# Optimization experiments

Hardware: AMD Instinct MI355X
Metric: run time of the kernel (lower is better)

Reference implementation:

```python
import jax, jax.numpy as jnp
import numpy as np

D_VOC, P_VOC, M_VOC = 2048, 1024, 4096
H = 256
T = 32
LD, LP, LM = 24, 12, 20


def _norm_adj(key, n):
    # binary graph + self loops, row-normalized (matches GCN.normalize(adj+I))
    a = (jax.random.uniform(key, (n, n)) < 0.002).astype(jnp.float32)
    a = a + jnp.eye(n, dtype=jnp.float32)
    rs = a.sum(axis=1)
    rinv = jnp.where(rs > 0, 1.0 / rs, 0.0)
    return rinv[:, None] * a


def setup_inputs() -> dict:
    key = jax.random.key(0)
    ks = jax.random.split(key, 32)
    s = float(1.0 / np.sqrt(H))
    u = lambda k, shape, sc: jax.random.uniform(k, shape, minval=-sc, maxval=sc, dtype=jnp.float32)
    inp = {
        'diag_codes': jax.random.randint(ks[0], (T, LD), 0, D_VOC),
        'proc_codes': jax.random.randint(ks[1], (T, LP), 0, P_VOC),
        'med_codes': jax.random.randint(ks[2], (T - 1, LM), 0, M_VOC),
        'diag_emb': u(ks[3], (D_VOC, H), 0.1),
        'proc_emb': u(ks[4], (P_VOC, H), 0.1),
        'gru_d_wih': u(ks[5], (3 * H, H), s), 'gru_d_whh': u(ks[6], (3 * H, H), s),
        'gru_d_bih': u(ks[7], (3 * H,), s), 'gru_d_bhh': u(ks[8], (3 * H,), s),
        'gru_p_wih': u(ks[9], (3 * H, H), s), 'gru_p_whh': u(ks[10], (3 * H, H), s),
        'gru_p_bih': u(ks[11], (3 * H,), s), 'gru_p_bhh': u(ks[12], (3 * H,), s),
        'q_w': u(ks[13], (2 * H, H), s), 'q_b': u(ks[14], (H,), s),
        'adj_ehr': _norm_adj(ks[15], M_VOC),
        'adj_ddi': _norm_adj(ks[16], M_VOC),
        'w1_ehr': u(ks[17], (M_VOC, H), s), 'b1_ehr': u(ks[18], (H,), s),
        'w2_ehr': u(ks[19], (H, H), s), 'b2_ehr': u(ks[20], (H,), s),
        'w1_ddi': u(ks[21], (M_VOC, H), s), 'b1_ddi': u(ks[22], (H,), s),
        'w2_ddi': u(ks[23], (H, H), s), 'b2_ddi': u(ks[24], (H,), s),
        'inter': jax.random.normal(ks[25], (1,), dtype=jnp.float32) / H,
        'proj_w': u(ks[26], (2 * H, H), s), 'proj_b': u(ks[27], (H,), s),
    }
    return inp


def _gru(x, wih, whh, bih, bhh):
    # torch.nn.GRU cell math; x: [T, H] -> outputs [T, H]
    def step(h, xt):
        gi = xt @ wih.T + bih
        gh = h @ whh.T + bhh
        ir, iz, inn = jnp.split(gi, 3)
        hr, hz, hn = jnp.split(gh, 3)
        r = jax.nn.sigmoid(ir + hr)
        z = jax.nn.sigmoid(iz + hz)
        n = jnp.tanh(inn + r * hn)
        h2 = (1.0 - z) * n + z * h
        return h2, h2
    _, ys = jax.lax.scan(step, jnp.zeros((x.shape[-1],), x.dtype), x)
    return ys


def _gcn(adj, w1, b1, w2, b2):
    # input features are identity, so first support mm(I, w1) == w1
    h1 = jax.nn.relu(adj @ w1 + b1)
    return adj @ (h1 @ w2) + b2


def reference(diag_codes, proc_codes, med_codes, diag_emb, proc_emb,
              gru_d_wih, gru_d_whh, gru_d_bih, gru_d_bhh,
              gru_p_wih, gru_p_whh, gru_p_bih, gru_p_bhh,
              q_w, q_b, adj_ehr, adj_ddi,
              w1_ehr, b1_ehr, w2_ehr, b2_ehr,
              w1_ddi, b1_ddi, w2_ddi, b2_ddi,
              inter, proj_w, proj_b):
    # ---- PatientEncoder: gather + sum codes per visit, GRU over visits ----
    seq_d = diag_emb[diag_codes].sum(axis=1)            # [T, H]
    seq_p = proc_emb[proc_codes].sum(axis=1)            # [T, H]
    od = _gru(seq_d, gru_d_wih, gru_d_whh, gru_d_bih, gru_d_bhh)
    op = _gru(seq_p, gru_p_wih, gru_p_whh, gru_p_bih, gru_p_bhh)
    feats = jnp.concatenate([od, op], axis=-1)          # [T, 2H]
    queries = jax.nn.relu(feats) @ q_w + q_b            # [T, H] (Sequential(ReLU, Linear))
    query = queries[-1:]                                # [1, H]
    history_keys = queries[:-1]                         # [T-1, H]
    # multi-hot history medication values (scatter)
    tm1 = med_codes.shape[0]
    history_values = jnp.zeros((tm1, M_VOC), jnp.float32).at[
        jnp.arange(tm1)[:, None], med_codes].set(1.0)   # [T-1, M_VOC]
    # ---- PriorEncoder ----
    prior = _gcn(adj_ehr, w1_ehr, b1_ehr, w2_ehr, b2_ehr) \
        - inter[0] * _gcn(adj_ddi, w1_ddi, b1_ddi, w2_ddi, b2_ddi)  # [M_VOC, H]
    w_emb = jax.nn.softmax(query @ prior.T, axis=-1)    # [1, M_VOC]
    # diag(w) @ prior == broadcast row-scale (the fused gather-weighted-scale)
    gc1 = w_emb.reshape(-1, 1) * prior                  # [M_VOC, H]
    visit_w = jax.nn.softmax(query @ history_keys.T, axis=-1)  # [1, T-1]
    wv = (visit_w @ history_values).reshape(-1, 1)      # [M_VOC, 1]
    gc2 = wv * prior                                    # [M_VOC, H]
    return jnp.concatenate([gc1, gc2], axis=-1) @ proj_w + proj_b  # [M_VOC, H]
```

## Files before the change

kernel.cpp:

```cpp
#include <hip/hip_runtime.h>
#include <hip/hip_bf16.h>

#define HD   256
#define TT   32
#define MV   4096
#define LD_  24
#define LP_  12
#define LM_  20
#define MAXNZ 96

typedef _Float16 h2v __attribute__((ext_vector_type(2)));
typedef _Float16 h8  __attribute__((ext_vector_type(8)));

__device__ __forceinline__ float fdot2(h2v a, h2v b, float c) {
#if __has_builtin(__builtin_amdgcn_fdot2)
  return __builtin_amdgcn_fdot2(a, b, c, false);
#else
  return c + (float)a[0] * (float)b[0] + (float)a[1] * (float)b[1];
#endif
}

#define PIN2(x) { float _t = __builtin_bit_cast(float, x); \
                  asm volatile("" : "+v"(_t));             \
                  x = __builtin_bit_cast(h2v, _t); }

__global__ __launch_bounds__(768) void k0_cvt(
    const float* __restrict__ whh_d, const float* __restrict__ whh_p,
    h8* __restrict__ wt)
{
  const int i = blockIdx.x, b = blockIdx.y, g = threadIdx.x;
  const float* whh = b ? whh_p : whh_d;
  const float* src = whh + (size_t)g * HD + 8 * i;
  h8 v;
#pragma unroll
  for (int e = 0; e < 8; ++e) v[e] = (_Float16)src[e];
  wt[((size_t)b * 32 + i) * 768 + g] = v;
}

__global__ __launch_bounds__(768) void k1_embed_gi(
    const int* __restrict__ dc, const int* __restrict__ pc,
    const float* __restrict__ demb, const float* __restrict__ pemb,
    const float* __restrict__ wih_d, const float* __restrict__ bih_d,
    const float* __restrict__ wih_p, const float* __restrict__ bih_p,
    float* __restrict__ GI)
{
  const int t = blockIdx.x, b = blockIdx.y;
  const int* codes = b ? pc : dc;
  const int L = b ? LP_ : LD_;
  const float* emb = b ? pemb : demb;
  const float* wih = b ? wih_p : wih_d;
  const float* bih = b ? bih_p : bih_d;
  __shared__ float s[HD];
  const int j = threadIdx.x;
  if (j < HD) {
    float acc = 0.f;
    for (int l = 0; l < L; ++l) acc += emb[(size_t)codes[t * L + l] * HD + j];
    s[j] = acc;
  }
  __syncthreads();
  const int g = j;
  float acc = bih[g];
  const float* wr = wih + (size_t)g * HD;
  for (int k = 0; k < HD; k += 4) {
    float4 w4 = *(const float4*)(wr + k);
    acc = fmaf(w4.x, s[k], acc);
    acc = fmaf(w4.y, s[k + 1], acc);
    acc = fmaf(w4.z, s[k + 2], acc);
    acc = fmaf(w4.w, s[k + 3], acc);
  }
  GI[((size_t)b * TT + t) * 768 + g] = acc;
}

__global__ __launch_bounds__(512)
__attribute__((amdgpu_waves_per_eu(2, 2)))
void k23_fused(
    const float* __restrict__ GI, const h8* __restrict__ wt,
    const float* __restrict__ bhh_d, const float* __restrict__ bhh_p,
    float* __restrict__ feats,
    const float* __restrict__ adj_e, const float* __restrict__ adj_d,
    int* __restrict__ cnt_g, int* __restrict__ cols_g,
    float* __restrict__ vals_g)
{
  __shared__ h8 hbuf[2][32];

  if (blockIdx.x < 2) {
    const int b = blockIdx.x, t = threadIdx.x;
    const int p = t >> 1;
    const int hk = t & 1;
    const float* gi = GI + (size_t)b * TT * 768;
    const float* bhh = b ? bhh_p : bhh_d;

    h2v w[192];
    {
      const h8* wbase = wt + (size_t)b * 32 * 768;
#pragma unroll
      for (int r3 = 0; r3 < 3; ++r3) {
#pragma unroll
        for (int ii = 0; ii < 16; ++ii) {
          union { h8 v; h2v q[4]; } u;
          u.v = wbase[(size_t)(hk * 16 + ii) * 768 + r3 * 256 + p];
          w[(r3 * 16 + ii) * 4 + 0] = u.q[0];
          w[(r3 * 16 + ii) * 4 + 1] = u.q[1];
          w[(r3 * 16 + ii) * 4 + 2] = u.q[2];
          w[(r3 * 16 + ii) * 4 + 3] = u.q[3];
        }
      }
    }
#pragma unroll
    for (int i = 0; i < 192; ++i) PIN2(w[i])

    const float bh_r = bhh[p], bh_z = bhh[256 + p], bh_n = bhh[512 + p];
    float hreg = 0.f;
    if (t < 256) ((_Float16*)&hbuf[0][0])[t] = (_Float16)0.f;
    __syncthreads();

    for (int tt = 0; tt < TT; ++tt) {
      const float* git = gi + tt * 768;
      float ir = 0.f, iz = 0.f, inn = 0.f;
      if (hk == 0) { ir = git[p]; iz = git[256 + p]; inn = git[512 + p]; }

      const h8* hb = hbuf[tt & 1];
      float dr0 = 0.f, dr1 = 0.f, dz0 = 0.f, dz1 = 0.f, dn0 = 0.f, dn1 = 0.f;
#pragma unroll
      for (int ii = 0; ii < 16; ++ii) {
        union { h8 v; h2v q[4]; } u;
        u.v = hb[hk * 16 + ii];
        dr0 = fdot2(w[(0 * 16 + ii) * 4 + 0], u.q[0], dr0);
        dr1 = fdot2(w[(0 * 16 + ii) * 4 + 1], u.q[1], dr1);
        dr0 = fdot2(w[(0 * 16 + ii) * 4 + 2], u.q[2], dr0);
        dr1 = fdot2(w[(0 * 16 + ii) * 4 + 3], u.q[3], dr1);
        dz0 = fdot2(w[(1 * 16 + ii) * 4 + 0], u.q[0], dz0);
        dz1 = fdot2(w[(1 * 16 + ii) * 4 + 1], u.q[1], dz1);
        dz0 = fdot2(w[(1 * 16 + ii) * 4 + 2], u.q[2], dz0);
        dz1 = fdot2(w[(1 * 16 + ii) * 4 + 3], u.q[3], dz1);
        dn0 = fdot2(w[(2 * 16 + ii) * 4 + 0], u.q[0], dn0);
        dn1 = fdot2(w[(2 * 16 + ii) * 4 + 1], u.q[1], dn1);
        dn0 = fdot2(w[(2 * 16 + ii) * 4 + 2], u.q[2], dn0);
        dn1 = fdot2(w[(2 * 16 + ii) * 4 + 3], u.q[3], dn1);
      }
      float dr = dr0 + dr1, dz = dz0 + dz1, dn = dn0 + dn1;
      dr += __shfl_xor(dr, 1, 64);
      dz += __shfl_xor(dz, 1, 64);
      dn += __shfl_xor(dn, 1, 64);
      if (hk == 0) {
        const float hr = dr + bh_r, hz = dz + bh_z, hn = dn + bh_n;
        const float r = 1.f / (1.f + __expf(-(ir + hr)));
        const float z = 1.f / (1.f + __expf(-(iz + hz)));
        const float n = tanhf(inn + r * hn);
        hreg = (1.f - z) * n + z * hreg;
        ((_Float16*)&hbuf[(tt & 1) ^ 1][0])[p] = (_Float16)hreg;
        feats[(size_t)tt * 512 + b * HD + p] = hreg;
      }
      __syncthreads();
    }
    return;
  }

  const int w = threadIdx.x >> 6, lane = threadIdx.x & 63;
  const int rg = (blockIdx.x - 2) * 8 + w;
  const int bsel = rg >> 12;
  const int r = rg & (MV - 1);
  const float* adj = (bsel ? adj_d : adj_e) + (size_t)r * MV;

  float4 ev[16];
#pragma unroll
  for (int c = 0; c < 16; ++c)
    ev[c] = *(const float4*)(adj + c * 256 + lane * 4);

  int cl = 0;
#pragma unroll
  for (int c = 0; c < 16; ++c)
    cl += (ev[c].x != 0.f) + (ev[c].y != 0.f) + (ev[c].z != 0.f) + (ev[c].w != 0.f);

  int pref = cl;
#pragma unroll
  for (int ofs = 1; ofs < 64; ofs <<= 1) {
    int v = __shfl_up(pref, ofs, 64);
    if (lane >= ofs) pref += v;
  }
  const int total = __shfl(pref, 63, 64);
  int pos = pref - cl;

  int* cg = cols_g + (size_t)rg * MAXNZ;
  float* vg = vals_g + (size_t)rg * MAXNZ;
#pragma unroll
  for (int c = 0; c < 16; ++c) {
    const float vv[4] = {ev[c].x, ev[c].y, ev[c].z, ev[c].w};
#pragma unroll
    for (int e = 0; e < 4; ++e) {
      if (vv[e] != 0.f) {
        if (pos < MAXNZ) { cg[pos] = c * 256 + lane * 4 + e; vg[pos] = vv[e]; }
        ++pos;
      }
    }
  }
  if (lane == 0) cnt_g[rg] = total > MAXNZ ? MAXNZ : total;
}

__global__ __launch_bounds__(256) void k2b_queries(
    const float* __restrict__ feats, const float* __restrict__ q_w,
    const float* __restrict__ q_b, float* __restrict__ queries)
{
  const int t = blockIdx.x, j = threadIdx.x;
  __shared__ float f[512];
  f[j] = fmaxf(feats[(size_t)t * 512 + j], 0.f);
  f[j + 256] = fmaxf(feats[(size_t)t * 512 + 256 + j], 0.f);
  __syncthreads();
  float acc = q_b[j];
  for (int k = 0; k < 512; ++k) acc = fmaf(f[k], q_w[(size_t)k * HD + j], acc);
  queries[(size_t)t * HD + j] = acc;
}

__global__ __launch_bounds__(512) void k45_z(
    const int* __restrict__ cnt_g, const int* __restrict__ cols_g,
    const float* __restrict__ vals_g,
    const float* __restrict__ w1_e, const float* __restrict__ b1_e,
    const float* __restrict__ w1_d, const float* __restrict__ b1_d,
    const float* __restrict__ w2_e, const float* __restrict__ w2_d,
    float* __restrict__ zz)
{
  const int blk = blockIdx.x, b = blockIdx.y;
  const int t = threadIdx.x;
  __shared__ float tile[8][HD];
  __shared__ float part[8][HD];

  {
    const int w = t >> 6, lane = t & 63;
    const int rg = b * MV + blk * 8 + w;
    const float* w1 = b ? w1_d : w1_e;
    const float* b1 = b ? b1_d : b1_e;
    const int n = cnt_g[rg];
    const int* cg = cols_g + (size_t)rg * MAXNZ;
    const float* vg = vals_g + (size_t)rg * MAXNZ;
    float4 acc = *(const float4*)(b1 + lane * 4);
    for (int k = 0; k < n; ++k) {
      const int col = cg[k];
      const float v = vg[k];
      const float4 wv4 = *(const float4*)(w1 + (size_t)col * HD + lane * 4);
      acc.x = fmaf(v, wv4.x, acc.x);
      acc.y = fmaf(v, wv4.y, acc.y);
      acc.z = fmaf(v, wv4.z, acc.z);
      acc.w = fmaf(v, wv4.w, acc.w);
    }
    float4* dst = (float4*)&tile[w][lane * 4];
    dst->x = fmaxf(acc.x, 0.f); dst->y = fmaxf(acc.y, 0.f);
    dst->z = fmaxf(acc.z, 0.f); dst->w = fmaxf(acc.w, 0.f);
  }
  __syncthreads();

  const int j = t & 255, half = t >> 8;
  const float* w2 = b ? w2_d : w2_e;
  float acc[8];
#pragma unroll
  for (int r = 0; r < 8; ++r) acc[r] = 0.f;
  const int k0 = half * 128;
  for (int k = k0; k < k0 + 128; k += 4) {
    float wa = w2[(size_t)(k + 0) * HD + j];
    float wb = w2[(size_t)(k + 1) * HD + j];
    float wc = w2[(size_t)(k + 2) * HD + j];
    float wd = w2[(size_t)(k + 3) * HD + j];
#pragma unroll
    for (int r = 0; r < 8; ++r) {
      float4 tv = *(const float4*)&tile[r][k];
      acc[r] = fmaf(tv.x, wa, acc[r]);
      acc[r] = fmaf(tv.y, wb, acc[r]);
      acc[r] = fmaf(tv.z, wc, acc[r]);
      acc[r] = fmaf(tv.w, wd, acc[r]);
    }
  }
  if (half == 1) {
#pragma unroll
    for (int r = 0; r < 8; ++r) part[r][j] = acc[r];
  }
  __syncthreads();
  if (half == 0) {
    float* zb = zz + (size_t)b * MV * HD + (size_t)blk * 8 * HD;
#pragma unroll
    for (int r = 0; r < 8; ++r) zb[r * HD + j] = acc[r] + part[r][j];
  }
}

__global__ __launch_bounds__(256) void k5_prior(
    const float* __restrict__ zz, const int* __restrict__ cnt_g,
    const int* __restrict__ cols_g, const float* __restrict__ vals_g,
    const float* __restrict__ b2_e, const float* __restrict__ b2_d,
    const float* __restrict__ inter, const float* __restrict__ queries,
    float* __restrict__ prior, float* __restrict__ s1)
{
  const int r = blockIdx.x, j = threadIdx.x;
  __shared__ float red[256];
  float acc_e = b2_e[j];
  {
    const int ne = cnt_g[r];
    const int* ce = cols_g + (size_t)r * MAXNZ;
    const float* ve = vals_g + (size_t)r * MAXNZ;
    for (int k = 0; k < ne; ++k)
      acc_e = fmaf(ve[k], zz[(size_t)ce[k] * HD + j], acc_e);
  }
  float acc_d = b2_d[j];
  {
    const int nd = cnt_g[MV + r];
    const int* cd = cols_g + (size_t)(MV + r) * MAXNZ;
    const float* vd = vals_g + (size_t)(MV + r) * MAXNZ;
    const float* zd = zz + (size_t)MV * HD;
    for (int k = 0; k < nd; ++k)
      acc_d = fmaf(vd[k], zd[(size_t)cd[k] * HD + j], acc_d);
  }
  const float pr = acc_e - inter[0] * acc_d;
  prior[(size_t)r * HD + j] = pr;
  red[j] = queries[31 * HD + j] * pr;
  __syncthreads();
  for (int s = 128; s > 0; s >>= 1) {
    if (j < s) red[j] += red[j + s];
    __syncthreads();
  }
  if (j == 0) s1[r] = red[0];
}

__global__ __launch_bounds__(1024) void k6a_softmax(
    const float* __restrict__ s1, const float* __restrict__ queries,
    float* __restrict__ w_emb, float* __restrict__ visw)
{
  const int j = threadIdx.x;
  __shared__ float red[1024];
  __shared__ float s2[31];
  float m = -1e30f;
  for (int i = j; i < MV; i += 1024) m = fmaxf(m, s1[i]);
  red[j] = m;
  __syncthreads();
  for (int s = 512; s > 0; s >>= 1) {
    if (j < s) red[j] = fmaxf(red[j], red[j + s]);
    __syncthreads();
  }
  const float mx = red[0];
  __syncthreads();
  float sum = 0.f;
  for (int i = j; i < MV; i += 1024) sum += __expf(s1[i] - mx);
  red[j] = sum;
  __syncthreads();
  for (int s = 512; s > 0; s >>= 1) {
    if (j < s) red[j] += red[j + s];
    __syncthreads();
  }
  const float inv = 1.f / red[0];
  for (int i = j; i < MV; i += 1024) w_emb[i] = __expf(s1[i] - mx) * inv;

  if (j < 31) {
    float acc = 0.f;
    for (int k = 0; k < HD; ++k)
      acc = fmaf(queries[31 * HD + k], queries[(size_t)j * HD + k], acc);
    s2[j] = acc;
  }
  __syncthreads();
  if (j == 0) {
    float mm = -1e30f;
    for (int t = 0; t < 31; ++t) mm = fmaxf(mm, s2[t]);
    float ss = 0.f;
    for (int t = 0; t < 31; ++t) ss += __expf(s2[t] - mm);
    const float is = 1.f / ss;
    for (int t = 0; t < 31; ++t) visw[t] = __expf(s2[t] - mm) * is;
  }
}

__global__ __launch_bounds__(1024) void k6b_wv(
    const int* __restrict__ med, const float* __restrict__ visw,
    float* __restrict__ wv)
{
  __shared__ int mc[31 * LM_];
  __shared__ float vw[31];
  const int j = threadIdx.x;
  if (j < 31 * LM_) mc[j] = med[j];
  if (j < 31) vw[j] = visw[j];
  __syncthreads();
  const int m = blockIdx.x * 1024 + j;
  float acc = 0.f;
  for (int t = 0; t < 31; ++t) {
    bool found = false;
#pragma unroll
    for (int l = 0; l < LM_; ++l) found = found || (mc[t * LM_ + l] == m);
    if (found) acc += vw[t];
  }
  wv[m] = acc;
}

__global__ __launch_bounds__(512) void k7_out(
    const float* __restrict__ prior, const float* __restrict__ w_emb,
    const float* __restrict__ wv, const float* __restrict__ proj_w,
    const float* __restrict__ proj_b, float* __restrict__ out)
{
  const int blk = blockIdx.x;
  const int t = threadIdx.x;
  const int j = t & 255, half = t >> 8;
  const int r0 = blk * 8;
  __shared__ float tile[8][HD];
  __shared__ float part[8][HD];
  __shared__ float we[8], wvv[8];
  {
    float4* t4 = (float4*)tile;
    const float4* s4 = (const float4*)(prior + (size_t)r0 * HD);
    t4[t] = s4[t];
  }
  if (t < 8) { we[t] = w_emb[r0 + t]; wvv[t] = wv[r0 + t]; }
  __syncthreads();
  const float* wmat = proj_w + (size_t)half * HD * HD;
  float acc[8];
#pragma unroll
  for (int r = 0; r < 8; ++r) acc[r] = 0.f;
  for (int k = 0; k < HD; k += 4) {
    float wa = wmat[(size_t)(k + 0) * HD + j];
    float wb = wmat[(size_t)(k + 1) * HD + j];
    float wc = wmat[(size_t)(k + 2) * HD + j];
    float wd = wmat[(size_t)(k + 3) * HD + j];
#pragma unroll
    for (int r = 0; r < 8; ++r) {
      float4 tv = *(const float4*)&tile[r][k];
      acc[r] = fmaf(tv.x, wa, acc[r]);
      acc[r] = fmaf(tv.y, wb, acc[r]);
      acc[r] = fmaf(tv.z, wc, acc[r]);
      acc[r] = fmaf(tv.w, wd, acc[r]);
    }
  }
  if (half == 1) {
#pragma unroll
    for (int r = 0; r < 8; ++r) part[r][j] = acc[r];
  }
  __syncthreads();
  if (half == 0) {
    const float pb = proj_b[j];
#pragma unroll
    for (int r = 0; r < 8; ++r)
      out[(size_t)(r0 + r) * HD + j] = we[r] * acc[r] + wvv[r] * part[r][j] + pb;
  }
}

extern "C" void kernel_launch(void* const* d_in, const int* in_sizes, int n_in,
                              void* d_out, int out_size, void* d_ws, size_t ws_size,
                              hipStream_t stream) {
  const int* diag_codes = (const int*)d_in[0];
  const int* proc_codes = (const int*)d_in[1];
  const int* med_codes  = (const int*)d_in[2];
  const float* diag_emb = (const float*)d_in[3];
  const float* proc_emb = (const float*)d_in[4];
  const float* wih_d = (const float*)d_in[5];
  const float* whh_d = (const float*)d_in[6];
  const float* bih_d = (const float*)d_in[7];
  const float* bhh_d = (const float*)d_in[8];
  const float* wih_p = (const float*)d_in[9];
  const float* whh_p = (const float*)d_in[10];
  const float* bih_p = (const float*)d_in[11];
  const float* bhh_p = (const float*)d_in[12];
  const float* q_w = (const float*)d_in[13];
  const float* q_b = (const float*)d_in[14];
  const float* adj_ehr = (const float*)d_in[15];
  const float* adj_ddi = (const float*)d_in[16];
  const float* w1_ehr = (const float*)d_in[17];
  const float* b1_ehr = (const float*)d_in[18];
  const float* w2_ehr = (const float*)d_in[19];
  const float* b2_ehr = (const float*)d_in[20];
  const float* w1_ddi = (const float*)d_in[21];
  const float* b1_ddi = (const float*)d_in[22];
  const float* w2_ddi = (const float*)d_in[23];
  const float* b2_ddi = (const float*)d_in[24];
  const float* inter = (const float*)d_in[25];
  const float* proj_w = (const float*)d_in[26];
  const float* proj_b = (const float*)d_in[27];
  float* out = (float*)d_out;

  float* ws = (float*)d_ws;
  size_t off = 0;
  float* GI      = ws + off; off += 2 * TT * 768;
  float* feats   = ws + off; off += TT * 512;
  float* queries = ws + off; off += TT * HD;
  float* zz      = ws + off; off += 2 * (size_t)MV * HD;
  float* prior   = ws + off; off += (size_t)MV * HD;
  float* s1      = ws + off; off += MV;
  float* w_emb   = ws + off; off += MV;
  float* visw    = ws + off; off += 32;
  float* wv      = ws + off; off += MV;
  int*   cnt_g   = (int*)(ws + off); off += 2 * MV;
  int*   cols_g  = (int*)(ws + off); off += 2 * (size_t)MV * MAXNZ;
  float* vals_g  = ws + off; off += 2 * (size_t)MV * MAXNZ;
  h8*    wt      = (h8*)(ws + off); off += 2 * 32 * 768 * 4;
  (void)ws_size; (void)in_sizes; (void)n_in; (void)out_size;

  k0_cvt<<<dim3(32, 2), 768, 0, stream>>>(whh_d, whh_p, wt);
  k1_embed_gi<<<dim3(TT, 2), 768, 0, stream>>>(diag_codes, proc_codes, diag_emb,
      proc_emb, wih_d, bih_d, wih_p, bih_p, GI);
  k23_fused<<<2 + 2 * MV / 8, 512, 0, stream>>>(GI, wt, bhh_d, bhh_p, feats,
      adj_ehr, adj_ddi, cnt_g, cols_g, vals_g);
  k2b_queries<<<TT, 256, 0, stream>>>(feats, q_w, q_b, queries);
  k45_z<<<dim3(MV / 8, 2), 512, 0, stream>>>(cnt_g, cols_g, vals_g,
      w1_ehr, b1_ehr, w1_ddi, b1_ddi, w2_ehr, w2_ddi, zz);
  k5_prior<<<MV, 256, 0, stream>>>(zz, cnt_g, cols_g, vals_g, b2_ehr, b2_ddi,
      inter, queries, prior, s1);
  k6a_softmax<<<1, 1024, 0, stream>>>(s1, queries, w_emb, visw);
  k6b_wv<<<MV / 1024, 1024, 0, stream>>>(med_codes, visw, wv);
  k7_out<<<MV / 8, 512, 0, stream>>>(prior, w_emb, wv, proj_w, proj_b, out);
}
```

Baseline: 206.5 us.

## Merge prep kernels and make adjacency-scan waves process multiple rows with double-buffered loads

Merges the weight-conversion and embedding/input-gate kernels into a single launch by branching on blockIdx.y. The adjacency compaction part of the fused GRU kernel now runs on 254 worker blocks instead of 1024. Each wave handles four or five rows with a stride of 2032 and alternates between two register buffers, so the next row's loads are in flight while the current row is compacted. This cuts launch overhead and the number of short-lived blocks, but doubles register use per wave and may reduce the memory parallelism available while the two GRU blocks run.

```diff
diff --git a/kernel.cpp b/kernel.cpp
--- a/kernel.cpp
+++ b/kernel.cpp
@@ -24,27 +24,26 @@
                   asm volatile("" : "+v"(_t));             \
                   x = __builtin_bit_cast(h2v, _t); }
 
-__global__ __launch_bounds__(768) void k0_cvt(
+__global__ __launch_bounds__(768) void k01_prep(
     const float* __restrict__ whh_d, const float* __restrict__ whh_p,
-    h8* __restrict__ wt)
-{
-  const int i = blockIdx.x, b = blockIdx.y, g = threadIdx.x;
-  const float* whh = b ? whh_p : whh_d;
-  const float* src = whh + (size_t)g * HD + 8 * i;
-  h8 v;
-#pragma unroll
-  for (int e = 0; e < 8; ++e) v[e] = (_Float16)src[e];
-  wt[((size_t)b * 32 + i) * 768 + g] = v;
-}
-
-__global__ __launch_bounds__(768) void k1_embed_gi(
+    h8* __restrict__ wt,
     const int* __restrict__ dc, const int* __restrict__ pc,
     const float* __restrict__ demb, const float* __restrict__ pemb,
     const float* __restrict__ wih_d, const float* __restrict__ bih_d,
     const float* __restrict__ wih_p, const float* __restrict__ bih_p,
     float* __restrict__ GI)
 {
-  const int t = blockIdx.x, b = blockIdx.y;
+  if (blockIdx.y < 2) {
+    const int i = blockIdx.x, b = blockIdx.y, g = threadIdx.x;
+    const float* whh = b ? whh_p : whh_d;
+    const float* src = whh + (size_t)g * HD + 8 * i;
+    h8 v;
+#pragma unroll
+    for (int e = 0; e < 8; ++e) v[e] = (_Float16)src[e];
+    wt[((size_t)b * 32 + i) * 768 + g] = v;
+    return;
+  }
+  const int t = blockIdx.x, b = blockIdx.y - 2;
   const int* codes = b ? pc : dc;
   const int L = b ? LP_ : LD_;
   const float* emb = b ? pemb : demb;
@@ -70,6 +69,45 @@
   }
   GI[((size_t)b * TT + t) * 768 + g] = acc;
 }
+
+#define LOADROW(EV, ADJROW)                                        \
+  _Pragma("unroll")                                                \
+  for (int c = 0; c < 16; ++c)                                     \
+    EV[c] = *(const float4*)((ADJROW) + c * 256 + lane * 4);
+
+#define PROCESS(EV, RG)                                                 \
+  {                                                                     \
+    int cl = 0;                                                         \
+    _Pragma("unroll")                                                   \
+    for (int c = 0; c < 16; ++c)                                        \
+      cl += (EV[c].x != 0.f) + (EV[c].y != 0.f) +                       \
+            (EV[c].z != 0.f) + (EV[c].w != 0.f);                        \
+    int pref = cl;                                                      \
+    _Pragma("unroll")                                                   \
+    for (int ofs = 1; ofs < 64; ofs <<= 1) {                            \
+      int v = __shfl_up(pref, ofs, 64);                                 \
+      if (lane >= ofs) pref += v;                                       \
+    }                                                                   \
+    const int total = __shfl(pref, 63, 64);                             \
+    int pos = pref - cl;                                                \
+    int* cg = cols_g + (size_t)(RG) * MAXNZ;                            \
+    float* vg = vals_g + (size_t)(RG) * MAXNZ;                          \
+    _Pragma("unroll")                                                   \
+    for (int c = 0; c < 16; ++c) {                                      \
+      const float vv[4] = {EV[c].x, EV[c].y, EV[c].z, EV[c].w};         \
+      _Pragma("unroll")                                                 \
+      for (int e = 0; e < 4; ++e) {                                     \
+        if (vv[e] != 0.f) {                                             \
+          if (pos < MAXNZ) { cg[pos] = c * 256 + lane * 4 + e;          \
+                             vg[pos] = vv[e]; }                         \
+          ++pos;                                                        \
+        }                                                               \
+      }                                                                 \
+    }                                                                   \
+    if (lane == 0) cnt_g[RG] = total > MAXNZ ? MAXNZ : total;           \
+  }
+
+#define ROWPTR(RG) (((RG) >> 12 ? adj_d : adj_e) + (size_t)((RG) & (MV - 1)) * MV)
 
 __global__ __launch_bounds__(512)
 __attribute__((amdgpu_waves_per_eu(2, 2)))
@@ -157,44 +195,22 @@
   }
 
   const int w = threadIdx.x >> 6, lane = threadIdx.x & 63;
-  const int rg = (blockIdx.x - 2) * 8 + w;
-  const int bsel = rg >> 12;
-  const int r = rg & (MV - 1);
-  const float* adj = (bsel ? adj_d : adj_e) + (size_t)r * MV;
-
-  float4 ev[16];
-#pragma unroll
-  for (int c = 0; c < 16; ++c)
-    ev[c] = *(const float4*)(adj + c * 256 + lane * 4);
-
-  int cl = 0;
-#pragma unroll
-  for (int c = 0; c < 16; ++c)
-    cl += (ev[c].x != 0.f) + (ev[c].y != 0.f) + (ev[c].z != 0.f) + (ev[c].w != 0.f);
-
-  int pref = cl;
-#pragma unroll
-  for (int ofs = 1; ofs < 64; ofs <<= 1) {
-    int v = __shfl_up(pref, ofs, 64);
-    if (lane >= ofs) pref += v;
-  }
-  const int total = __shfl(pref, 63, 64);
-  int pos = pref - cl;
-
-  int* cg = cols_g + (size_t)rg * MAXNZ;
-  float* vg = vals_g + (size_t)rg * MAXNZ;
-#pragma unroll
-  for (int c = 0; c < 16; ++c) {
-    const float vv[4] = {ev[c].x, ev[c].y, ev[c].z, ev[c].w};
-#pragma unroll
-    for (int e = 0; e < 4; ++e) {
-      if (vv[e] != 0.f) {
-        if (pos < MAXNZ) { cg[pos] = c * 256 + lane * 4 + e; vg[pos] = vv[e]; }
-        ++pos;
-      }
-    }
-  }
-  if (lane == 0) cnt_g[rg] = total > MAXNZ ? MAXNZ : total;
+  const int rg0 = (blockIdx.x - 2) * 8 + w;
+  const int r0 = rg0, r1 = rg0 + 2032, r2 = rg0 + 4064, r3 = rg0 + 6096,
+            r4 = rg0 + 8128;
+  const bool has5 = (r4 < 2 * MV);
+
+  float4 evA[16], evB[16];
+  LOADROW(evA, ROWPTR(r0))
+  LOADROW(evB, ROWPTR(r1))
+  PROCESS(evA, r0)
+  LOADROW(evA, ROWPTR(r2))
+  PROCESS(evB, r1)
+  LOADROW(evB, ROWPTR(r3))
+  PROCESS(evA, r2)
+  if (has5) { LOADROW(evA, ROWPTR(r4)) }
+  PROCESS(evB, r3)
+  if (has5) { PROCESS(evA, r4) }
 }
 
 __global__ __launch_bounds__(256) void k2b_queries(
@@ -483,10 +499,10 @@
   h8*    wt      = (h8*)(ws + off); off += 2 * 32 * 768 * 4;
   (void)ws_size; (void)in_sizes; (void)n_in; (void)out_size;
 
-  k0_cvt<<<dim3(32, 2), 768, 0, stream>>>(whh_d, whh_p, wt);
-  k1_embed_gi<<<dim3(TT, 2), 768, 0, stream>>>(diag_codes, proc_codes, diag_emb,
-      proc_emb, wih_d, bih_d, wih_p, bih_p, GI);
-  k23_fused<<<2 + 2 * MV / 8, 512, 0, stream>>>(GI, wt, bhh_d, bhh_p, feats,
+  k01_prep<<<dim3(32, 4), 768, 0, stream>>>(whh_d, whh_p, wt,
+      diag_codes, proc_codes, diag_emb, proc_emb,
+      wih_d, bih_d, wih_p, bih_p, GI);
+  k23_fused<<<256, 512, 0, stream>>>(GI, wt, bhh_d, bhh_p, feats,
       adj_ehr, adj_ddi, cnt_g, cols_g, vals_g);
   k2b_queries<<<TT, 256, 0, stream>>>(feats, q_w, q_b, queries);
   k45_z<<<dim3(MV / 8, 2), 512, 0, stream>>>(cnt_g, cols_g, vals_g,
```

Measured after the change: 205.7 us. Within noise of the previous version (-0.4%).

## Merge prep kernels, widen GRU blocks to 1024 threads, fold wv into output kernel

Applied to the files above, without the earlier changes.

Combines the weight fp16 conversion and embedding/input-gate kernels into one launch, and folds the history multi-hot weighting (wv) into the final projection kernel, removing two launches and the wv buffer. The fused GRU/adjacency kernel now uses 1024-thread blocks: the GRU splits each hidden unit's dot product over 4 lanes instead of 2, halving per-thread register weights, and each adjacency block handles 16 rows. The aim is to shorten the serial GRU critical path and cut launch overhead. The cost is an extra shuffle stage per step and redundant med-code loads in every k7 block.

```diff
diff --git a/kernel.cpp b/kernel.cpp
--- a/kernel.cpp
+++ b/kernel.cpp
@@ -24,27 +24,26 @@
                   asm volatile("" : "+v"(_t));             \
                   x = __builtin_bit_cast(h2v, _t); }
 
-__global__ __launch_bounds__(768) void k0_cvt(
+__global__ __launch_bounds__(768) void k01_prep(
     const float* __restrict__ whh_d, const float* __restrict__ whh_p,
-    h8* __restrict__ wt)
-{
-  const int i = blockIdx.x, b = blockIdx.y, g = threadIdx.x;
-  const float* whh = b ? whh_p : whh_d;
-  const float* src = whh + (size_t)g * HD + 8 * i;
-  h8 v;
-#pragma unroll
-  for (int e = 0; e < 8; ++e) v[e] = (_Float16)src[e];
-  wt[((size_t)b * 32 + i) * 768 + g] = v;
-}
-
-__global__ __launch_bounds__(768) void k1_embed_gi(
+    h8* __restrict__ wt,
     const int* __restrict__ dc, const int* __restrict__ pc,
     const float* __restrict__ demb, const float* __restrict__ pemb,
     const float* __restrict__ wih_d, const float* __restrict__ bih_d,
     const float* __restrict__ wih_p, const float* __restrict__ bih_p,
     float* __restrict__ GI)
 {
-  const int t = blockIdx.x, b = blockIdx.y;
+  if (blockIdx.y < 2) {
+    const int i = blockIdx.x, b = blockIdx.y, g = threadIdx.x;
+    const float* whh = b ? whh_p : whh_d;
+    const float* src = whh + (size_t)g * HD + 8 * i;
+    h8 v;
+#pragma unroll
+    for (int e = 0; e < 8; ++e) v[e] = (_Float16)src[e];
+    wt[((size_t)b * 32 + i) * 768 + g] = v;
+    return;
+  }
+  const int t = blockIdx.x, b = blockIdx.y - 2;
   const int* codes = b ? pc : dc;
   const int L = b ? LP_ : LD_;
   const float* emb = b ? pemb : demb;
@@ -71,8 +70,8 @@
   GI[((size_t)b * TT + t) * 768 + g] = acc;
 }
 
-__global__ __launch_bounds__(512)
-__attribute__((amdgpu_waves_per_eu(2, 2)))
+__global__ __launch_bounds__(1024)
+__attribute__((amdgpu_waves_per_eu(4, 4)))
 void k23_fused(
     const float* __restrict__ GI, const h8* __restrict__ wt,
     const float* __restrict__ bhh_d, const float* __restrict__ bhh_p,
@@ -85,29 +84,29 @@
 
   if (blockIdx.x < 2) {
     const int b = blockIdx.x, t = threadIdx.x;
-    const int p = t >> 1;
-    const int hk = t & 1;
+    const int p = t >> 2;
+    const int qk = t & 3;
     const float* gi = GI + (size_t)b * TT * 768;
     const float* bhh = b ? bhh_p : bhh_d;
 
-    h2v w[192];
+    h2v w[96];
     {
       const h8* wbase = wt + (size_t)b * 32 * 768;
 #pragma unroll
       for (int r3 = 0; r3 < 3; ++r3) {
 #pragma unroll
-        for (int ii = 0; ii < 16; ++ii) {
+        for (int ii = 0; ii < 8; ++ii) {
           union { h8 v; h2v q[4]; } u;
-          u.v = wbase[(size_t)(hk * 16 + ii) * 768 + r3 * 256 + p];
-          w[(r3 * 16 + ii) * 4 + 0] = u.q[0];
-          w[(r3 * 16 + ii) * 4 + 1] = u.q[1];
-          w[(r3 * 16 + ii) * 4 + 2] = u.q[2];
-          w[(r3 * 16 + ii) * 4 + 3] = u.q[3];
+          u.v = wbase[(size_t)(qk * 8 + ii) * 768 + r3 * 256 + p];
+          w[(r3 * 8 + ii) * 4 + 0] = u.q[0];
+          w[(r3 * 8 + ii) * 4 + 1] = u.q[1];
+          w[(r3 * 8 + ii) * 4 + 2] = u.q[2];
+          w[(r3 * 8 + ii) * 4 + 3] = u.q[3];
         }
       }
     }
 #pragma unroll
-    for (int i = 0; i < 192; ++i) PIN2(w[i])
+    for (int i = 0; i < 96; ++i) PIN2(w[i])
 
     const float bh_r = bhh[p], bh_z = bhh[256 + p], bh_n = bhh[512 + p];
     float hreg = 0.f;
@@ -117,32 +116,32 @@
     for (int tt = 0; tt < TT; ++tt) {
       const float* git = gi + tt * 768;
       float ir = 0.f, iz = 0.f, inn = 0.f;
-      if (hk == 0) { ir = git[p]; iz = git[256 + p]; inn = git[512 + p]; }
+      if (qk == 0) { ir = git[p]; iz = git[256 + p]; inn = git[512 + p]; }
 
       const h8* hb = hbuf[tt & 1];
       float dr0 = 0.f, dr1 = 0.f, dz0 = 0.f, dz1 = 0.f, dn0 = 0.f, dn1 = 0.f;
 #pragma unroll
-      for (int ii = 0; ii < 16; ++ii) {
+      for (int ii = 0; ii < 8; ++ii) {
         union { h8 v; h2v q[4]; } u;
-        u.v = hb[hk * 16 + ii];
-        dr0 = fdot2(w[(0 * 16 + ii) * 4 + 0], u.q[0], dr0);
-        dr1 = fdot2(w[(0 * 16 + ii) * 4 + 1], u.q[1], dr1);
-        dr0 = fdot2(w[(0 * 16 + ii) * 4 + 2], u.q[2], dr0);
-        dr1 = fdot2(w[(0 * 16 + ii) * 4 + 3], u.q[3], dr1);
-        dz0 = fdot2(w[(1 * 16 + ii) * 4 + 0], u.q[0], dz0);
-        dz1 = fdot2(w[(1 * 16 + ii) * 4 + 1], u.q[1], dz1);
-        dz0 = fdot2(w[(1 * 16 + ii) * 4 + 2], u.q[2], dz0);
-        dz1 = fdot2(w[(1 * 16 + ii) * 4 + 3], u.q[3], dz1);
-        dn0 = fdot2(w[(2 * 16 + ii) * 4 + 0], u.q[0], dn0);
-        dn1 = fdot2(w[(2 * 16 + ii) * 4 + 1], u.q[1], dn1);
-        dn0 = fdot2(w[(2 * 16 + ii) * 4 + 2], u.q[2], dn0);
-        dn1 = fdot2(w[(2 * 16 + ii) * 4 + 3], u.q[3], dn1);
+        u.v = hb[qk * 8 + ii];
+        dr0 = fdot2(w[(0 * 8 + ii) * 4 + 0], u.q[0], dr0);
+        dr1 = fdot2(w[(0 * 8 + ii) * 4 + 1], u.q[1], dr1);
+        dr0 = fdot2(w[(0 * 8 + ii) * 4 + 2], u.q[2], dr0);
+        dr1 = fdot2(w[(0 * 8 + ii) * 4 + 3], u.q[3], dr1);
+        dz0 = fdot2(w[(1 * 8 + ii) * 4 + 0], u.q[0], dz0);
+        dz1 = fdot2(w[(1 * 8 + ii) * 4 + 1], u.q[1], dz1);
+        dz0 = fdot2(w[(1 * 8 + ii) * 4 + 2], u.q[2], dz0);
+        dz1 = fdot2(w[(1 * 8 + ii) * 4 + 3], u.q[3], dz1);
+        dn0 = fdot2(w[(2 * 8 + ii) * 4 + 0], u.q[0], dn0);
+        dn1 = fdot2(w[(2 * 8 + ii) * 4 + 1], u.q[1], dn1);
+        dn0 = fdot2(w[(2 * 8 + ii) * 4 + 2], u.q[2], dn0);
+        dn1 = fdot2(w[(2 * 8 + ii) * 4 + 3], u.q[3], dn1);
       }
       float dr = dr0 + dr1, dz = dz0 + dz1, dn = dn0 + dn1;
-      dr += __shfl_xor(dr, 1, 64);
-      dz += __shfl_xor(dz, 1, 64);
-      dn += __shfl_xor(dn, 1, 64);
-      if (hk == 0) {
+      dr += __shfl_xor(dr, 1, 64); dr += __shfl_xor(dr, 2, 64);
+      dz += __shfl_xor(dz, 1, 64); dz += __shfl_xor(dz, 2, 64);
+      dn += __shfl_xor(dn, 1, 64); dn += __shfl_xor(dn, 2, 64);
+      if (qk == 0) {
         const float hr = dr + bh_r, hz = dz + bh_z, hn = dn + bh_n;
         const float r = 1.f / (1.f + __expf(-(ir + hr)));
         const float z = 1.f / (1.f + __expf(-(iz + hz)));
@@ -157,7 +156,7 @@
   }
 
   const int w = threadIdx.x >> 6, lane = threadIdx.x & 63;
-  const int rg = (blockIdx.x - 2) * 8 + w;
+  const int rg = (blockIdx.x - 2) * 16 + w;
   const int bsel = rg >> 12;
   const int r = rg & (MV - 1);
   const float* adj = (bsel ? adj_d : adj_e) + (size_t)r * MV;
@@ -362,31 +361,11 @@
   }
 }
 
-__global__ __launch_bounds__(1024) void k6b_wv(
-    const int* __restrict__ med, const float* __restrict__ visw,
-    float* __restrict__ wv)
-{
-  __shared__ int mc[31 * LM_];
-  __shared__ float vw[31];
-  const int j = threadIdx.x;
-  if (j < 31 * LM_) mc[j] = med[j];
-  if (j < 31) vw[j] = visw[j];
-  __syncthreads();
-  const int m = blockIdx.x * 1024 + j;
-  float acc = 0.f;
-  for (int t = 0; t < 31; ++t) {
-    bool found = false;
-#pragma unroll
-    for (int l = 0; l < LM_; ++l) found = found || (mc[t * LM_ + l] == m);
-    if (found) acc += vw[t];
-  }
-  wv[m] = acc;
-}
-
 __global__ __launch_bounds__(512) void k7_out(
     const float* __restrict__ prior, const float* __restrict__ w_emb,
-    const float* __restrict__ wv, const float* __restrict__ proj_w,
-    const float* __restrict__ proj_b, float* __restrict__ out)
+    const float* __restrict__ visw, const int* __restrict__ med,
+    const float* __restrict__ proj_w, const float* __restrict__ proj_b,
+    float* __restrict__ out)
 {
   const int blk = blockIdx.x;
   const int t = threadIdx.x;
@@ -395,13 +374,31 @@
   __shared__ float tile[8][HD];
   __shared__ float part[8][HD];
   __shared__ float we[8], wvv[8];
+  __shared__ int mc[31 * LM_];
   {
     float4* t4 = (float4*)tile;
     const float4* s4 = (const float4*)(prior + (size_t)r0 * HD);
     t4[t] = s4[t];
   }
-  if (t < 8) { we[t] = w_emb[r0 + t]; wvv[t] = wv[r0 + t]; }
-  __syncthreads();
+  for (int i = t; i < 31 * LM_; i += 512) mc[i] = med[i];
+  if (t < 8) we[t] = w_emb[r0 + t];
+  __syncthreads();
+
+  if (half == 0) {
+    const int r = j >> 5, tp = j & 31;
+    float contrib = 0.f;
+    if (tp < 31) {
+      const int m = r0 + r;
+      bool found = false;
+#pragma unroll
+      for (int l = 0; l < LM_; ++l) found = found || (mc[tp * LM_ + l] == m);
+      if (found) contrib = visw[tp];
+    }
+#pragma unroll
+    for (int msk = 16; msk > 0; msk >>= 1) contrib += __shfl_xor(contrib, msk, 32);
+    if (tp == 0) wvv[r] = contrib;
+  }
+
   const float* wmat = proj_w + (size_t)half * HD * HD;
   float acc[8];
 #pragma unroll
@@ -476,17 +473,16 @@
   float* s1      = ws + off; off += MV;
   float* w_emb   = ws + off; off += MV;
   float* visw    = ws + off; off += 32;
-  float* wv      = ws + off; off += MV;
   int*   cnt_g   = (int*)(ws + off); off += 2 * MV;
   int*   cols_g  = (int*)(ws + off); off += 2 * (size_t)MV * MAXNZ;
   float* vals_g  = ws + off; off += 2 * (size_t)MV * MAXNZ;
   h8*    wt      = (h8*)(ws + off); off += 2 * 32 * 768 * 4;
   (void)ws_size; (void)in_sizes; (void)n_in; (void)out_size;
 
-  k0_cvt<<<dim3(32, 2), 768, 0, stream>>>(whh_d, whh_p, wt);
-  k1_embed_gi<<<dim3(TT, 2), 768, 0, stream>>>(diag_codes, proc_codes, diag_emb,
-      proc_emb, wih_d, bih_d, wih_p, bih_p, GI);
-  k23_fused<<<2 + 2 * MV / 8, 512, 0, stream>>>(GI, wt, bhh_d, bhh_p, feats,
+  k01_prep<<<dim3(32, 4), 768, 0, stream>>>(whh_d, whh_p, wt,
+      diag_codes, proc_codes, diag_emb, proc_emb,
+      wih_d, bih_d, wih_p, bih_p, GI);
+  k23_fused<<<2 + 512, 1024, 0, stream>>>(GI, wt, bhh_d, bhh_p, feats,
       adj_ehr, adj_ddi, cnt_g, cols_g, vals_g);
   k2b_queries<<<TT, 256, 0, stream>>>(feats, q_w, q_b, queries);
   k45_z<<<dim3(MV / 8, 2), 512, 0, stream>>>(cnt_g, cols_g, vals_g,
@@ -494,6 +490,6 @@
   k5_prior<<<MV, 256, 0, stream>>>(zz, cnt_g, cols_g, vals_g, b2_ehr, b2_ddi,
       inter, queries, prior, s1);
   k6a_softmax<<<1, 1024, 0, stream>>>(s1, queries, w_emb, visw);
-  k6b_wv<<<MV / 1024, 1024, 0, stream>>>(med_codes, visw, wv);
-  k7_out<<<MV / 8, 512, 0, stream>>>(prior, w_emb, wv, proj_w, proj_b, out);
-}
+  k7_out<<<MV / 8, 512, 0, stream>>>(prior, w_emb, visw, med_codes,
+      proj_w, proj_b, out);
+}
```

After: 203.3 us. Within noise of the previous version (-1.6%).
